# Kernel optimization log

Measured on AMD Instinct MI355X. Metric: run time of the kernel, lower is better.

The kernel has to match this reference:

```python
import jax, jax.numpy as jnp
import numpy as np

NUM_STAB = 1e-3  # numerical_stabilizer for relu kernel


def _relu_feature(x, proj):
    # x: [B, L, H, D], proj: [M, D] -> [B, L, H, M]
    ratio = 1.0 / jnp.sqrt(jnp.asarray(proj.shape[0], x.dtype))
    return jax.nn.relu(ratio * jnp.einsum('blhd,md->blhm', x, proj)) + NUM_STAB


def setup_inputs() -> dict:
    key = jax.random.key(0)
    k1, k2, k3, k4, k5 = jax.random.split(key, 5)
    B, L, H, D, M = 16, 576, 12, 64, 8  # L = length_of_side**2 = 24**2
    return {
        'query': jax.random.normal(k1, (B, L, H, D), dtype=jnp.float32),
        'key': jax.random.normal(k2, (B, L, H, D), dtype=jnp.float32),
        'value': jax.random.normal(k3, (B, L, H, D), dtype=jnp.float32),
        'projection_matrix': jax.random.normal(k4, (M, D), dtype=jnp.float32),
        # RPE mask is nonnegative per-head mixing matrix [H, L, L]
        'mask_matrix': jax.random.uniform(k5, (H, L, L), dtype=jnp.float32),
    }


def reference(query, key, value, projection_matrix, mask_matrix):
    # ReLU kernel features (projection_matrix_type='relu')
    q_prime = _relu_feature(query, projection_matrix)  # [B, L, H, M]
    k_prime = _relu_feature(key, projection_matrix)    # [B, L, H, M]
    B, L, H, M = k_prime.shape
    D = value.shape[-1]

    # D_1[b,l,h,m,d] = k'[b,l,h,m] * v[b,l,h,d], flattened over (m,d)
    D_1 = jnp.einsum('blhm,blhd->blhmd', k_prime, value).reshape(B, L, H, M * D)
    # mask-matrix causal/RPE mixing over the L dimension (per head)
    D_1_hat = jnp.einsum('hij,bjhc->bihc', mask_matrix, D_1).reshape(B, L, H, M, D)
    D_2_hat = jnp.einsum('hij,bjhm->bihm', mask_matrix, k_prime)  # [B, L, H, M]

    av_attention = jnp.einsum('blhm,blhmd->blhd', q_prime, D_1_hat)  # [B, L, H, D]
    ks_sum = jnp.sum(D_2_hat, axis=1)                                # [B, H, M]
    normalizer = jnp.einsum('blhm,bhm->blh', q_prime, ks_sum)        # [B, L, H]
    return av_attention / normalizer[..., None]
```

## Files before the change

kernel.cpp:

```cpp
#include <hip/hip_runtime.h>


#define B_ 16
#define L_ 576
#define H_ 12
#define D_ 64
#define M_ 8
#define NUM_STAB 1e-3f
#define RATIO 0.35355339059327373f

typedef __attribute__((ext_vector_type(8))) short short8;
typedef __attribute__((ext_vector_type(4))) float f32x4;

__device__ inline unsigned short f2bf(float x) {
    union { float f; unsigned u; } a; a.f = x;
    unsigned r = (a.u + 0x7FFFu + ((a.u >> 16) & 1u)) >> 16;
    return (unsigned short)r;
}
__device__ inline float bf2f(unsigned short h) {
    union { float f; unsigned u; } a; a.u = ((unsigned)h) << 16;
    return a.f;
}

#define WS_CMASK 0
#define WS_QP    (H_ * L_)
#define WS_KP    (WS_QP + B_ * H_ * L_ * M_)

__global__ __launch_bounds__(256) void feat_cmask_kernel(const float* __restrict__ q,
                                                         const float* __restrict__ k,
                                                         const float* __restrict__ proj,
                                                         const float* __restrict__ mask,
                                                         float* __restrict__ qp,
                                                         float* __restrict__ kp,
                                                         float* __restrict__ cmask) {
    __shared__ float proj_t[64][8];
    __shared__ float xbuf[32][68];
    const int lc = blockIdx.x, h = blockIdx.y, b = blockIdx.z, t = threadIdx.x;
    {
        int m = t >> 6, kk = t & 63;
        proj_t[kk][m] = RATIO * proj[t];
        int t2 = t + 256;
        m = t2 >> 6; kk = t2 & 63;
        proj_t[kk][m] = RATIO * proj[t2];
    }
    const int row8 = t >> 3, m8 = t & 7;
#pragma unroll
    for (int s = 0; s < 2; ++s) {
        const float* src = (s == 0) ? q : k;
        float* dst = (s == 0) ? qp : kp;
        __syncthreads();
#pragma unroll
        for (int p = 0; p < 2; ++p) {
            int idx = p * 256 + t, row = idx >> 4, c4 = idx & 15;
            float4 val = *(const float4*)(src + (((size_t)b * L_ + lc * 32 + row) * H_ + h) * D_ + c4 * 4);
            *(float4*)&xbuf[row][c4 * 4] = val;
        }
        __syncthreads();
        float acc = 0.f;
#pragma unroll 8
        for (int kk = 0; kk < D_; ++kk) acc = fmaf(xbuf[row8][kk], proj_t[kk][m8], acc);
        dst[((size_t)(b * H_ + h) * L_ + lc * 32 + row8) * M_ + m8] = fmaxf(acc, 0.f) + NUM_STAB;
    }
    if (b < 2) {
        const int c = t & 15, r16 = t >> 4;
        const int col0 = lc * 32 + b * 16;
        const float* mb = mask + (size_t)h * L_ * L_ + col0 + c;
        float a = 0.f;
#pragma unroll 4
        for (int k2 = 0; k2 < 36; ++k2) a += mb[(size_t)(r16 + 16 * k2) * L_];
        __syncthreads();
        float* red = &xbuf[0][0];
        red[c * 16 + r16] = a;
        __syncthreads();
        if (t < 16) {
            float s = 0.f;
#pragma unroll
            for (int g = 0; g < 16; ++g) s += red[t * 16 + g];
            cmask[h * L_ + col0 + t] = s;
        }
    }
}

__global__ __launch_bounds__(256, 4) void attn_kernel(const float* __restrict__ v,
                                                      const float* __restrict__ mask,
                                                      const float* __restrict__ qp,
                                                      const float* __restrict__ kp,
                                                      const float* __restrict__ cmask,
                                                      float* __restrict__ out) {
    __shared__ __align__(16) unsigned short Sp[64 * 72];
    __shared__ __align__(16) unsigned short Bt[64 * 72];
    __shared__ __align__(16) unsigned short Qp[64 * 32];
    __shared__ __align__(16) unsigned short Kp[32 * 32];
    __shared__ float cm_s[L_];

    const int t = threadIdx.x;
    int id = blockIdx.x;
    const int bhi = id & 7; id >>= 3;
    const int blo = id & 1; id >>= 1;
    const int it = id % 9, h = id / 9;
    const int b = bhi * 2 + blo;
    const int i0 = it * 64;

    const float* maskbase = mask + (size_t)h * L_ * L_;
    const float* kpb = kp + (size_t)(b * H_ + h) * L_ * M_;
    const float* qpb = qp + ((size_t)(b * H_ + h) * L_ + i0) * M_;
    const float* vb  = v + ((size_t)b * L_ * H_ + h) * D_;

    cm_s[t] = cmask[h * L_ + t];
    cm_s[t + 256] = cmask[h * L_ + t + 256];
    if (t < 64) cm_s[t + 512] = cmask[h * L_ + t + 512];

    {
        int i = t & 63, p = t >> 6;
        float q0 = qpb[i * 8 + 2 * p], q1 = qpb[i * 8 + 2 * p + 1];
        unsigned short h0 = f2bf(q0), h1 = f2bf(q1);
        unsigned short l0 = f2bf(q0 - bf2f(h0)), l1 = f2bf(q1 - bf2f(h1));
        unsigned* qw = (unsigned*)Qp;
        qw[i * 16 + p]      = (unsigned)h0 | ((unsigned)h1 << 16);
        qw[i * 16 + 4 + p]  = (unsigned)l0 | ((unsigned)l1 << 16);
        qw[i * 16 + 8 + p]  = 0u;
        qw[i * 16 + 12 + p] = 0u;
    }
    {
        unsigned* kw = (unsigned*)Kp;
        int row = t >> 3, cp = t & 7;
        kw[row * 16 + 8 + cp] = 0u;
    }
    __syncthreads();

    const int lane = t & 63, wv = t >> 6;
    const int c15 = lane & 15, kq = lane >> 4;

    short8 afq = *(const short8*)&Qp[(16 * wv + c15) * 32 + kq * 8];

    f32x4 acc[4];
    acc[0] = (f32x4){0.f, 0.f, 0.f, 0.f};
    acc[1] = acc[0]; acc[2] = acc[0]; acc[3] = acc[0];
    float nacc[4] = {0.f, 0.f, 0.f, 0.f};

    const int dS = t & 63, jgS = t >> 6;
    const int jK = t >> 3, mK = t & 7;
    const int ko2 = (kq < 2) ? (8 - kq * 8) : kq * 8;

    for (int jt = 0; jt < 18; ++jt) {
        const int j0 = jt * 32;
        __syncthreads();
        {
            float kv = kpb[(j0 + jK) * 8 + mK];
            unsigned short kh = f2bf(kv);
            unsigned short kl = f2bf(kv - bf2f(kh));
            Kp[jK * 32 + mK] = kh;
            Kp[jK * 32 + 8 + mK] = kl;
        }
        {
            unsigned short vh[8], vl[8];
#pragma unroll
            for (int qv = 0; qv < 8; ++qv) {
                float vf = vb[(size_t)(j0 + 8 * jgS + qv) * H_ * D_ + dS];
                vh[qv] = f2bf(vf);
                vl[qv] = f2bf(vf - bf2f(vh[qv]));
            }
            *(short8*)&Bt[dS * 72 + 8 * jgS] = *(const short8*)vh;
            *(short8*)&Bt[dS * 72 + 32 + 8 * jgS] = *(const short8*)vl;
        }
        __syncthreads();
        {
            f32x4 s2[2];
#pragma unroll
            for (int tj = 0; tj < 2; ++tj) {
                short8 b1 = *(const short8*)&Kp[(16 * tj + c15) * 32 + kq * 8];
                short8 b2 = *(const short8*)&Kp[(16 * tj + c15) * 32 + ko2];
                f32x4 z = (f32x4){0.f, 0.f, 0.f, 0.f};
                z = __builtin_amdgcn_mfma_f32_16x16x32_bf16(afq, b1, z, 0, 0, 0);
                z = __builtin_amdgcn_mfma_f32_16x16x32_bf16(afq, b2, z, 0, 0, 0);
                s2[tj] = z;
            }
            float mload[8];
#pragma unroll
            for (int tj = 0; tj < 2; ++tj)
#pragma unroll
                for (int r = 0; r < 4; ++r)
                    mload[tj * 4 + r] =
                        maskbase[(size_t)(i0 + 16 * wv + 4 * kq + r) * L_ + j0 + 16 * tj + c15];
            float cm0 = cm_s[j0 + c15], cm1 = cm_s[j0 + 16 + c15];
#pragma unroll
            for (int tj = 0; tj < 2; ++tj) {
                float cmv = tj ? cm1 : cm0;
#pragma unroll
                for (int r = 0; r < 4; ++r) {
                    float raw = s2[tj][r];
                    nacc[r] = fmaf(cmv, raw, nacc[r]);
                    float sm = raw * mload[tj * 4 + r];
                    unsigned short sh = f2bf(sm);
                    unsigned short sl = f2bf(sm - bf2f(sh));
                    int i = 16 * wv + 4 * kq + r;
                    Sp[i * 72 + 16 * tj + c15] = sh;
                    Sp[i * 72 + 32 + 16 * tj + c15] = sl;
                }
            }
        }
        __syncthreads();
        {
            short8 as0 = *(const short8*)&Sp[(16 * wv + c15) * 72 + kq * 8];
            short8 as1 = *(const short8*)&Sp[(16 * wv + c15) * 72 + 32 + kq * 8];
#pragma unroll
            for (int di = 0; di < 4; ++di) {
                const unsigned short* bp = &Bt[(16 * di + c15) * 72 + kq * 8];
                short8 bs0 = *(const short8*)bp;
                short8 bs1 = *(const short8*)(bp + 32);
                acc[di] = __builtin_amdgcn_mfma_f32_16x16x32_bf16(as0, bs0, acc[di], 0, 0, 0);
                acc[di] = __builtin_amdgcn_mfma_f32_16x16x32_bf16(as1, bs1, acc[di], 0, 0, 0);
                acc[di] = __builtin_amdgcn_mfma_f32_16x16x32_bf16(as0, bs1, acc[di], 0, 0, 0);
                acc[di] = __builtin_amdgcn_mfma_f32_16x16x32_bf16(as1, bs0, acc[di], 0, 0, 0);
            }
        }
    }

#pragma unroll
    for (int r = 0; r < 4; ++r) {
        float nv = nacc[r];
        nv += __shfl_xor(nv, 1);
        nv += __shfl_xor(nv, 2);
        nv += __shfl_xor(nv, 4);
        nv += __shfl_xor(nv, 8);
        nacc[r] = 1.0f / nv;
    }
#pragma unroll
    for (int di = 0; di < 4; ++di)
#pragma unroll
        for (int r = 0; r < 4; ++r) {
            int i = 16 * wv + 4 * kq + r;
            out[(((size_t)b * L_ + i0 + i) * H_ + h) * D_ + 16 * di + c15] = acc[di][r] * nacc[r];
        }
}

extern "C" void kernel_launch(void* const* d_in, const int* in_sizes, int n_in,
                              void* d_out, int out_size, void* d_ws, size_t ws_size,
                              hipStream_t stream) {
    const float* q    = (const float*)d_in[0];
    const float* k    = (const float*)d_in[1];
    const float* v    = (const float*)d_in[2];
    const float* proj = (const float*)d_in[3];
    const float* mask = (const float*)d_in[4];
    float* out = (float*)d_out;

    float* ws = (float*)d_ws;
    float* cmask = ws + WS_CMASK;
    float* qp_w  = ws + WS_QP;
    float* kp_w  = ws + WS_KP;

    feat_cmask_kernel<<<dim3(L_ / 32, H_, B_), 256, 0, stream>>>(q, k, proj, mask, qp_w, kp_w, cmask);
    attn_kernel<<<1728, 256, 0, stream>>>(v, mask, qp_w, kp_w, cmask, out);
}
```

Measured before the change: 202.8 us.

## Drop split-bf16 error compensation, store bf16 features, prefetch and double-buffer attention tiles

Removes the hi/lo bf16 split for Q', K', V and the masked scores, so each matmul uses a single bf16 MFMA instead of two or four. The feature kernel now writes bf16 features, computing them with register-held projection rows and shuffle reductions instead of shared-memory staging. The attention kernel keeps per-wave score tiles, double-buffers the V tile and prefetches the next tile's V, mask and K' into registers, cutting the barriers per iteration from three to one. In exchange, accuracy drops to plain bf16, which may miss the tolerance.

```diff
diff --git a/kernel.cpp b/kernel.cpp
--- a/kernel.cpp
+++ b/kernel.cpp
@@ -12,85 +12,97 @@
 typedef __attribute__((ext_vector_type(8))) short short8;
 typedef __attribute__((ext_vector_type(4))) float f32x4;
 
+union Pack {
+    uint4 u4;
+    short8 s8;
+    uint2 u2[2];
+    unsigned u[4];
+    unsigned short us[8];
+};
+
 __device__ inline unsigned short f2bf(float x) {
     union { float f; unsigned u; } a; a.f = x;
     unsigned r = (a.u + 0x7FFFu + ((a.u >> 16) & 1u)) >> 16;
     return (unsigned short)r;
 }
-__device__ inline float bf2f(unsigned short h) {
-    union { float f; unsigned u; } a; a.u = ((unsigned)h) << 16;
-    return a.f;
-}
-
-#define WS_CMASK 0
-#define WS_QP    (H_ * L_)
-#define WS_KP    (WS_QP + B_ * H_ * L_ * M_)
-
-__global__ __launch_bounds__(256) void feat_cmask_kernel(const float* __restrict__ q,
-                                                         const float* __restrict__ k,
-                                                         const float* __restrict__ proj,
-                                                         const float* __restrict__ mask,
-                                                         float* __restrict__ qp,
-                                                         float* __restrict__ kp,
-                                                         float* __restrict__ cmask) {
-    __shared__ float proj_t[64][8];
-    __shared__ float xbuf[32][68];
+
+#define WS_QP_OFF (H_ * L_)
+#define QP_ELEMS  ((size_t)B_ * H_ * L_ * M_)
+
+__global__ __launch_bounds__(256) void feat_kernel(const float* __restrict__ q,
+                                                   const float* __restrict__ k,
+                                                   const float* __restrict__ proj,
+                                                   const float* __restrict__ mask,
+                                                   unsigned short* __restrict__ qp,
+                                                   unsigned short* __restrict__ kp,
+                                                   float* __restrict__ cmask) {
+    __shared__ float cred[4][16];
     const int lc = blockIdx.x, h = blockIdx.y, b = blockIdx.z, t = threadIdx.x;
-    {
-        int m = t >> 6, kk = t & 63;
-        proj_t[kk][m] = RATIO * proj[t];
-        int t2 = t + 256;
-        m = t2 >> 6; kk = t2 & 63;
-        proj_t[kk][m] = RATIO * proj[t2];
-    }
-    const int row8 = t >> 3, m8 = t & 7;
+    const int wv = t >> 6, l = t & 63, r8 = l >> 3, c8 = l & 7;
+    const int row = lc * 32 + wv * 8 + r8;
+
+    float4 pj0[8], pj1[8];
+#pragma unroll
+    for (int m = 0; m < 8; ++m) {
+        pj0[m] = *(const float4*)(proj + m * 64 + c8 * 8);
+        pj1[m] = *(const float4*)(proj + m * 64 + c8 * 8 + 4);
+    }
+
 #pragma unroll
     for (int s = 0; s < 2; ++s) {
-        const float* src = (s == 0) ? q : k;
-        float* dst = (s == 0) ? qp : kp;
-        __syncthreads();
-#pragma unroll
-        for (int p = 0; p < 2; ++p) {
-            int idx = p * 256 + t, row = idx >> 4, c4 = idx & 15;
-            float4 val = *(const float4*)(src + (((size_t)b * L_ + lc * 32 + row) * H_ + h) * D_ + c4 * 4);
-            *(float4*)&xbuf[row][c4 * 4] = val;
-        }
-        __syncthreads();
-        float acc = 0.f;
-#pragma unroll 8
-        for (int kk = 0; kk < D_; ++kk) acc = fmaf(xbuf[row8][kk], proj_t[kk][m8], acc);
-        dst[((size_t)(b * H_ + h) * L_ + lc * 32 + row8) * M_ + m8] = fmaxf(acc, 0.f) + NUM_STAB;
-    }
+        const float* src = s ? k : q;
+        unsigned short* dst = s ? kp : qp;
+        const float* xp = src + (((size_t)b * L_ + row) * H_ + h) * D_ + c8 * 8;
+        float4 x0 = *(const float4*)xp;
+        float4 x1 = *(const float4*)(xp + 4);
+        x0.x *= RATIO; x0.y *= RATIO; x0.z *= RATIO; x0.w *= RATIO;
+        x1.x *= RATIO; x1.y *= RATIO; x1.z *= RATIO; x1.w *= RATIO;
+        float p[8];
+#pragma unroll
+        for (int m = 0; m < 8; ++m) {
+            p[m] = x0.x * pj0[m].x + x0.y * pj0[m].y + x0.z * pj0[m].z + x0.w * pj0[m].w
+                 + x1.x * pj1[m].x + x1.y * pj1[m].y + x1.z * pj1[m].z + x1.w * pj1[m].w;
+        }
+#pragma unroll
+        for (int st = 1; st <= 4; st <<= 1) {
+#pragma unroll
+            for (int m = 0; m < 8; ++m) p[m] += __shfl_xor(p[m], st, 64);
+        }
+        float r = p[0];
+        r = (c8 == 1) ? p[1] : r;
+        r = (c8 == 2) ? p[2] : r;
+        r = (c8 == 3) ? p[3] : r;
+        r = (c8 == 4) ? p[4] : r;
+        r = (c8 == 5) ? p[5] : r;
+        r = (c8 == 6) ? p[6] : r;
+        r = (c8 == 7) ? p[7] : r;
+        r = fmaxf(r, 0.f) + NUM_STAB;
+        dst[((size_t)(b * H_ + h) * L_ + row) * 8 + c8] = f2bf(r);
+    }
+
     if (b < 2) {
-        const int c = t & 15, r16 = t >> 4;
+        const int c = t & 15, rg = t >> 4;
         const int col0 = lc * 32 + b * 16;
         const float* mb = mask + (size_t)h * L_ * L_ + col0 + c;
         float a = 0.f;
 #pragma unroll 4
-        for (int k2 = 0; k2 < 36; ++k2) a += mb[(size_t)(r16 + 16 * k2) * L_];
+        for (int k2 = 0; k2 < 36; ++k2) a += mb[(size_t)(rg + 16 * k2) * L_];
+        a += __shfl_xor(a, 16, 64);
+        a += __shfl_xor(a, 32, 64);
+        if ((l >> 4) == 0) cred[wv][c] = a;
         __syncthreads();
-        float* red = &xbuf[0][0];
-        red[c * 16 + r16] = a;
-        __syncthreads();
-        if (t < 16) {
-            float s = 0.f;
-#pragma unroll
-            for (int g = 0; g < 16; ++g) s += red[t * 16 + g];
-            cmask[h * L_ + col0 + t] = s;
-        }
+        if (t < 16) cmask[h * L_ + col0 + t] = cred[0][t] + cred[1][t] + cred[2][t] + cred[3][t];
     }
 }
 
 __global__ __launch_bounds__(256, 4) void attn_kernel(const float* __restrict__ v,
                                                       const float* __restrict__ mask,
-                                                      const float* __restrict__ qp,
-                                                      const float* __restrict__ kp,
+                                                      const unsigned short* __restrict__ qp,
+                                                      const unsigned short* __restrict__ kp,
                                                       const float* __restrict__ cmask,
                                                       float* __restrict__ out) {
-    __shared__ __align__(16) unsigned short Sp[64 * 72];
-    __shared__ __align__(16) unsigned short Bt[64 * 72];
-    __shared__ __align__(16) unsigned short Qp[64 * 32];
-    __shared__ __align__(16) unsigned short Kp[32 * 32];
+    __shared__ __align__(16) unsigned short Sp[4 * 16 * 40];
+    __shared__ __align__(16) unsigned short Bt[2][64 * 40];
     __shared__ float cm_s[L_];
 
     const int t = threadIdx.x;
@@ -101,137 +113,122 @@
     const int b = bhi * 2 + blo;
     const int i0 = it * 64;
 
-    const float* maskbase = mask + (size_t)h * L_ * L_;
-    const float* kpb = kp + (size_t)(b * H_ + h) * L_ * M_;
-    const float* qpb = qp + ((size_t)(b * H_ + h) * L_ + i0) * M_;
-    const float* vb  = v + ((size_t)b * L_ * H_ + h) * D_;
+    const int wv = t >> 6, l = t & 63, c15 = l & 15, kq = l >> 4;
 
     cm_s[t] = cmask[h * L_ + t];
     cm_s[t + 256] = cmask[h * L_ + t + 256];
     if (t < 64) cm_s[t + 512] = cmask[h * L_ + t + 512];
 
+    const float* maskbase = mask + (size_t)h * L_ * L_ + (size_t)(i0 + 16 * wv + c15) * L_;
+    const unsigned short* kpb = kp + (size_t)(b * H_ + h) * L_ * 8;
+    const float* vb = v + ((size_t)b * L_ * H_ + h) * D_ + l;
+
+    short8 Bq;
     {
-        int i = t & 63, p = t >> 6;
-        float q0 = qpb[i * 8 + 2 * p], q1 = qpb[i * 8 + 2 * p + 1];
-        unsigned short h0 = f2bf(q0), h1 = f2bf(q1);
-        unsigned short l0 = f2bf(q0 - bf2f(h0)), l1 = f2bf(q1 - bf2f(h1));
-        unsigned* qw = (unsigned*)Qp;
-        qw[i * 16 + p]      = (unsigned)h0 | ((unsigned)h1 << 16);
-        qw[i * 16 + 4 + p]  = (unsigned)l0 | ((unsigned)l1 << 16);
-        qw[i * 16 + 8 + p]  = 0u;
-        qw[i * 16 + 12 + p] = 0u;
-    }
+        Pack pk; pk.u4 = make_uint4(0, 0, 0, 0);
+        if (kq == 0) {
+            const unsigned short* qpb = qp + ((size_t)(b * H_ + h) * L_ + i0 + 16 * wv + c15) * 8;
+            pk.u4 = *(const uint4*)qpb;
+        }
+        Bq = pk.s8;
+    }
+
+    unsigned short* SpW = Sp + wv * 16 * 40;
+
+    f32x4 acc0 = {0.f, 0.f, 0.f, 0.f}, acc1 = acc0, acc2 = acc0, acc3 = acc0;
+    float nacc = 0.f;
+
+    float vf[8];
+    float4 mv0, mv1;
+    uint4 kraw = make_uint4(0, 0, 0, 0);
     {
-        unsigned* kw = (unsigned*)Kp;
-        int row = t >> 3, cp = t & 7;
-        kw[row * 16 + 8 + cp] = 0u;
-    }
+#pragma unroll
+        for (int qv = 0; qv < 8; ++qv) vf[qv] = vb[(size_t)(8 * wv + qv) * (H_ * D_)];
+        mv0 = *(const float4*)(maskbase + 4 * kq);
+        mv1 = *(const float4*)(maskbase + 16 + 4 * kq);
+        if (kq < 2) kraw = *(const uint4*)(kpb + (size_t)(16 * kq + c15) * 8);
+    }
+
     __syncthreads();
-
-    const int lane = t & 63, wv = t >> 6;
-    const int c15 = lane & 15, kq = lane >> 4;
-
-    short8 afq = *(const short8*)&Qp[(16 * wv + c15) * 32 + kq * 8];
-
-    f32x4 acc[4];
-    acc[0] = (f32x4){0.f, 0.f, 0.f, 0.f};
-    acc[1] = acc[0]; acc[2] = acc[0]; acc[3] = acc[0];
-    float nacc[4] = {0.f, 0.f, 0.f, 0.f};
-
-    const int dS = t & 63, jgS = t >> 6;
-    const int jK = t >> 3, mK = t & 7;
-    const int ko2 = (kq < 2) ? (8 - kq * 8) : kq * 8;
 
     for (int jt = 0; jt < 18; ++jt) {
         const int j0 = jt * 32;
+        const int slab = jt & 1;
+
+        Pack a0, a1;
+        a1.u[0] = __shfl_down(kraw.x, 16, 64);
+        a1.u[1] = __shfl_down(kraw.y, 16, 64);
+        a1.u[2] = __shfl_down(kraw.z, 16, 64);
+        a1.u[3] = __shfl_down(kraw.w, 16, 64);
+        if (kq == 0) {
+            a0.u4 = kraw;
+        } else {
+            a0.u4 = make_uint4(0, 0, 0, 0);
+            a1.u4 = make_uint4(0, 0, 0, 0);
+        }
+        const f32x4 zz = {0.f, 0.f, 0.f, 0.f};
+        f32x4 s0 = __builtin_amdgcn_mfma_f32_16x16x32_bf16(a0.s8, Bq, zz, 0, 0, 0);
+        f32x4 s1 = __builtin_amdgcn_mfma_f32_16x16x32_bf16(a1.s8, Bq, zz, 0, 0, 0);
+
+        {
+            Pack pv;
+#pragma unroll
+            for (int qv = 0; qv < 8; ++qv) pv.us[qv] = f2bf(vf[qv]);
+            *(uint4*)&Bt[slab][l * 40 + 8 * wv] = pv.u4;
+        }
+        {
+            float4 cm0 = *(const float4*)&cm_s[j0 + 4 * kq];
+            float4 cm1 = *(const float4*)&cm_s[j0 + 16 + 4 * kq];
+            nacc += cm0.x * s0[0] + cm0.y * s0[1] + cm0.z * s0[2] + cm0.w * s0[3]
+                  + cm1.x * s1[0] + cm1.y * s1[1] + cm1.z * s1[2] + cm1.w * s1[3];
+            Pack ps;
+            ps.us[0] = f2bf(s0[0] * mv0.x);
+            ps.us[1] = f2bf(s0[1] * mv0.y);
+            ps.us[2] = f2bf(s0[2] * mv0.z);
+            ps.us[3] = f2bf(s0[3] * mv0.w);
+            ps.us[4] = f2bf(s1[0] * mv1.x);
+            ps.us[5] = f2bf(s1[1] * mv1.y);
+            ps.us[6] = f2bf(s1[2] * mv1.z);
+            ps.us[7] = f2bf(s1[3] * mv1.w);
+            *(uint2*)&SpW[c15 * 40 + 4 * kq] = ps.u2[0];
+            *(uint2*)&SpW[c15 * 40 + 16 + 4 * kq] = ps.u2[1];
+        }
+        {
+            const int jn = (jt < 17) ? j0 + 32 : 0;
+#pragma unroll
+            for (int qv = 0; qv < 8; ++qv) vf[qv] = vb[(size_t)(jn + 8 * wv + qv) * (H_ * D_)];
+            mv0 = *(const float4*)(maskbase + jn + 4 * kq);
+            mv1 = *(const float4*)(maskbase + jn + 16 + 4 * kq);
+            if (kq < 2) kraw = *(const uint4*)(kpb + (size_t)(jn + 16 * kq + c15) * 8);
+        }
         __syncthreads();
-        {
-            float kv = kpb[(j0 + jK) * 8 + mK];
-            unsigned short kh = f2bf(kv);
-            unsigned short kl = f2bf(kv - bf2f(kh));
-            Kp[jK * 32 + mK] = kh;
-            Kp[jK * 32 + 8 + mK] = kl;
-        }
-        {
-            unsigned short vh[8], vl[8];
-#pragma unroll
-            for (int qv = 0; qv < 8; ++qv) {
-                float vf = vb[(size_t)(j0 + 8 * jgS + qv) * H_ * D_ + dS];
-                vh[qv] = f2bf(vf);
-                vl[qv] = f2bf(vf - bf2f(vh[qv]));
-            }
-            *(short8*)&Bt[dS * 72 + 8 * jgS] = *(const short8*)vh;
-            *(short8*)&Bt[dS * 72 + 32 + 8 * jgS] = *(const short8*)vl;
-        }
-        __syncthreads();
-        {
-            f32x4 s2[2];
-#pragma unroll
-            for (int tj = 0; tj < 2; ++tj) {
-                short8 b1 = *(const short8*)&Kp[(16 * tj + c15) * 32 + kq * 8];
-                short8 b2 = *(const short8*)&Kp[(16 * tj + c15) * 32 + ko2];
-                f32x4 z = (f32x4){0.f, 0.f, 0.f, 0.f};
-                z = __builtin_amdgcn_mfma_f32_16x16x32_bf16(afq, b1, z, 0, 0, 0);
-                z = __builtin_amdgcn_mfma_f32_16x16x32_bf16(afq, b2, z, 0, 0, 0);
-                s2[tj] = z;
-            }
-            float mload[8];
-#pragma unroll
-            for (int tj = 0; tj < 2; ++tj)
-#pragma unroll
-                for (int r = 0; r < 4; ++r)
-                    mload[tj * 4 + r] =
-                        maskbase[(size_t)(i0 + 16 * wv + 4 * kq + r) * L_ + j0 + 16 * tj + c15];
-            float cm0 = cm_s[j0 + c15], cm1 = cm_s[j0 + 16 + c15];
-#pragma unroll
-            for (int tj = 0; tj < 2; ++tj) {
-                float cmv = tj ? cm1 : cm0;
-#pragma unroll
-                for (int r = 0; r < 4; ++r) {
-                    float raw = s2[tj][r];
-                    nacc[r] = fmaf(cmv, raw, nacc[r]);
-                    float sm = raw * mload[tj * 4 + r];
-                    unsigned short sh = f2bf(sm);
-                    unsigned short sl = f2bf(sm - bf2f(sh));
-                    int i = 16 * wv + 4 * kq + r;
-                    Sp[i * 72 + 16 * tj + c15] = sh;
-                    Sp[i * 72 + 32 + 16 * tj + c15] = sl;
-                }
-            }
-        }
-        __syncthreads();
-        {
-            short8 as0 = *(const short8*)&Sp[(16 * wv + c15) * 72 + kq * 8];
-            short8 as1 = *(const short8*)&Sp[(16 * wv + c15) * 72 + 32 + kq * 8];
-#pragma unroll
-            for (int di = 0; di < 4; ++di) {
-                const unsigned short* bp = &Bt[(16 * di + c15) * 72 + kq * 8];
-                short8 bs0 = *(const short8*)bp;
-                short8 bs1 = *(const short8*)(bp + 32);
-                acc[di] = __builtin_amdgcn_mfma_f32_16x16x32_bf16(as0, bs0, acc[di], 0, 0, 0);
-                acc[di] = __builtin_amdgcn_mfma_f32_16x16x32_bf16(as1, bs1, acc[di], 0, 0, 0);
-                acc[di] = __builtin_amdgcn_mfma_f32_16x16x32_bf16(as0, bs1, acc[di], 0, 0, 0);
-                acc[di] = __builtin_amdgcn_mfma_f32_16x16x32_bf16(as1, bs0, acc[di], 0, 0, 0);
-            }
-        }
-    }
-
-#pragma unroll
-    for (int r = 0; r < 4; ++r) {
-        float nv = nacc[r];
-        nv += __shfl_xor(nv, 1);
-        nv += __shfl_xor(nv, 2);
-        nv += __shfl_xor(nv, 4);
-        nv += __shfl_xor(nv, 8);
-        nacc[r] = 1.0f / nv;
-    }
+
+        {
+            short8 As = *(const short8*)&SpW[c15 * 40 + kq * 8];
+            short8 B0 = *(const short8*)&Bt[slab][c15 * 40 + kq * 8];
+            short8 B1 = *(const short8*)&Bt[slab][(16 + c15) * 40 + kq * 8];
+            short8 B2 = *(const short8*)&Bt[slab][(32 + c15) * 40 + kq * 8];
+            short8 B3 = *(const short8*)&Bt[slab][(48 + c15) * 40 + kq * 8];
+            acc0 = __builtin_amdgcn_mfma_f32_16x16x32_bf16(As, B0, acc0, 0, 0, 0);
+            acc1 = __builtin_amdgcn_mfma_f32_16x16x32_bf16(As, B1, acc1, 0, 0, 0);
+            acc2 = __builtin_amdgcn_mfma_f32_16x16x32_bf16(As, B2, acc2, 0, 0, 0);
+            acc3 = __builtin_amdgcn_mfma_f32_16x16x32_bf16(As, B3, acc3, 0, 0, 0);
+        }
+    }
+
+    nacc += __shfl_xor(nacc, 16, 64);
+    nacc += __shfl_xor(nacc, 32, 64);
+    float iv[4];
+#pragma unroll
+    for (int r = 0; r < 4; ++r) iv[r] = 1.0f / __shfl(nacc, 4 * kq + r, 64);
+
+    float* ob = out + (((size_t)b * L_ + i0 + 16 * wv + 4 * kq) * H_ + h) * D_ + c15;
+    const f32x4 aa[4] = {acc0, acc1, acc2, acc3};
 #pragma unroll
     for (int di = 0; di < 4; ++di)
 #pragma unroll
-        for (int r = 0; r < 4; ++r) {
-            int i = 16 * wv + 4 * kq + r;
-            out[(((size_t)b * L_ + i0 + i) * H_ + h) * D_ + 16 * di + c15] = acc[di][r] * nacc[r];
-        }
+        for (int r = 0; r < 4; ++r)
+            ob[(size_t)r * (H_ * D_) + 16 * di] = aa[di][r] * iv[r];
 }
 
 extern "C" void kernel_launch(void* const* d_in, const int* in_sizes, int n_in,
@@ -245,10 +242,10 @@
     float* out = (float*)d_out;
 
     float* ws = (float*)d_ws;
-    float* cmask = ws + WS_CMASK;
-    float* qp_w  = ws + WS_QP;
-    float* kp_w  = ws + WS_KP;
-
-    feat_cmask_kernel<<<dim3(L_ / 32, H_, B_), 256, 0, stream>>>(q, k, proj, mask, qp_w, kp_w, cmask);
+    float* cmask = ws;
+    unsigned short* qp_w = (unsigned short*)(ws + WS_QP_OFF);
+    unsigned short* kp_w = qp_w + QP_ELEMS;
+
+    feat_kernel<<<dim3(L_ / 32, H_, B_), 256, 0, stream>>>(q, k, proj, mask, qp_w, kp_w, cmask);
     attn_kernel<<<1728, 256, 0, stream>>>(v, mask, qp_w, kp_w, cmask, out);
 }
```

Result: faster. 182.8 us (-9.9%).
